# Optimization experiments

Hardware: AMD Instinct MI355X
Metric: run time of the kernel (lower is better)

Reference implementation:

```python
import jax, jax.numpy as jnp
import numpy as np

B, N, D = 2, 2048, 2048
H = 16
HD = D // H  # 128


def setup_inputs() -> dict:
    key = jax.random.key(0)
    k1, k2, k3 = jax.random.split(key, 3)
    x = jax.random.normal(k1, (B, N, D), dtype=jnp.float32)
    # Linear weights stored as [in, out] so y = x @ W matches torch's x @ W.T
    Wq = jax.random.normal(k2, (D, D), dtype=jnp.float32) * (D ** -0.5)
    Wo = jax.random.normal(k3, (D, D), dtype=jnp.float32) * (D ** -0.5)
    bo = jnp.zeros((D,), dtype=jnp.float32)
    return {"x": x, "Wq": Wq, "Wo": Wo, "bo": bo}


def reference(x, Wq, Wo, bo):
    # NOTE: source module (faithfully) projects q, k, v all with q_matrix.
    b, n, d = x.shape
    q = x @ Wq                                   # [B, N, D]
    qh = q.reshape(b, n, H, HD).transpose(0, 2, 1, 3)  # [B, H, N, HD]
    scores = jnp.einsum("bhnd,bhmd->bhnm", qh, qh) * (HD ** -0.5)  # [B,H,N,N]
    attn = jax.nn.softmax(scores, axis=-1)
    y = jnp.einsum("bhnm,bhmd->bhnd", attn, qh)  # [B, H, N, HD]
    y = y.transpose(0, 2, 1, 3).reshape(b, n, d)  # [B, N, D]
    return y @ Wo + bo
```

## Files before the change

kernel.cpp:

```cpp
#include <hip/hip_runtime.h>
#include <hip/hip_bf16.h>

#define BATCH 2
#define SEQ   2048
#define DIM   2048
#define NHEAD 16
#define HDIM  128

#define KSTRIDE 136
#define VSTRIDE 72
#define PSTRIDE 72

typedef __bf16 bf16;
typedef __attribute__((ext_vector_type(2))) __bf16 bf16x2;
typedef __attribute__((ext_vector_type(4))) __bf16 bf16x4;
typedef __attribute__((ext_vector_type(8))) __bf16 bf16x8;
typedef __attribute__((ext_vector_type(4))) float f32x4;

__device__ __forceinline__ void load_lds16(const bf16* g, bf16* l) {
    __builtin_amdgcn_global_load_lds((const __attribute__((address_space(1))) void*)g,
                                     (__attribute__((address_space(3))) void*)l, 16, 0, 0);
}

__device__ __forceinline__ float exp2_hw(float x) { return __builtin_amdgcn_exp2f(x); }

__global__ __launch_bounds__(256)
void cvt_bf16(const float* __restrict__ x, bf16* __restrict__ xb, int n4)
{
    const int i = blockIdx.x * 256 + threadIdx.x;
    if (i < n4) {
        const float4 f = ((const float4*)x)[i];
        ((bf16x4*)xb)[i] = (bf16x4){(bf16)f.x, (bf16)f.y, (bf16)f.z, (bf16)f.w};
    }
}

__global__ __launch_bounds__(256)
void transpose_w(const float* __restrict__ W, bf16* __restrict__ Wt)
{
    __shared__ bf16 T[64 * 72];
    const int kb = blockIdx.y * 64, nb = blockIdx.x * 64;

    const int a = threadIdx.x & 31;
    const int g = threadIdx.x >> 5;

    {
        const float* s0 = W + (size_t)(kb + 2 * a) * DIM + nb + g * 8;
        const float4 r0a = *(const float4*)(s0);
        const float4 r0b = *(const float4*)(s0 + 4);
        const float4 r1a = *(const float4*)(s0 + DIM);
        const float4 r1b = *(const float4*)(s0 + DIM + 4);
        float v0[8] = {r0a.x, r0a.y, r0a.z, r0a.w, r0b.x, r0b.y, r0b.z, r0b.w};
        float v1[8] = {r1a.x, r1a.y, r1a.z, r1a.w, r1b.x, r1b.y, r1b.z, r1b.w};
        #pragma unroll
        for (int i = 0; i < 8; ++i)
            *(bf16x2*)&T[(g * 8 + i) * 72 + 2 * a] = (bf16x2){(bf16)v0[i], (bf16)v1[i]};
    }
    __syncthreads();

    const int r  = threadIdx.x >> 2;
    const int k0 = (threadIdx.x & 3) * 16;
    bf16x8 o0 = *(const bf16x8*)&T[r * 72 + k0];
    bf16x8 o1 = *(const bf16x8*)&T[r * 72 + k0 + 8];
    *(bf16x8*)(Wt + (size_t)(nb + r) * DIM + kb + k0)     = o0;
    *(bf16x8*)(Wt + (size_t)(nb + r) * DIM + kb + k0 + 8) = o1;
}

template<bool OUT_F32_BIAS>
__global__ __launch_bounds__(256)
void gemm_bt(const bf16* __restrict__ A, const bf16* __restrict__ Bt,
             const float* __restrict__ bias, void* __restrict__ Cptr,
             int M, int N, int K)
{
    __shared__ bf16 As[2][128 * 32];
    __shared__ bf16 Bs[2][128 * 32];

    const int tid  = threadIdx.x;
    const int wave = tid >> 6;
    const int lane = tid & 63;
    const int quad = lane >> 4;
    const int l16  = lane & 15;
    const int wr   = (wave >> 1) * 64;
    const int wc   = (wave & 1) * 64;
    const int rowBase = blockIdx.y * 128;
    const int colBase = blockIdx.x * 128;

    const int srow = lane >> 2;
    const int scol = (lane & 3) * 8;
    const bf16* aBase = A  + (size_t)(rowBase + wave * 16 + srow) * K + scol;
    const bf16* bBase = Bt + (size_t)(colBase + wave * 16 + srow) * K + scol;

    f32x4 acc[4][4] = {};

    for (int k0 = 0; k0 < K; k0 += 64) {
        #pragma unroll
        for (int rh = 0; rh < 2; ++rh) {
            #pragma unroll
            for (int kh = 0; kh < 2; ++kh) {
                load_lds16(aBase + (size_t)rh * 64 * K + k0 + kh * 32,
                           (bf16*)As[kh] + (rh * 64 + wave * 16) * 32);
                load_lds16(bBase + (size_t)rh * 64 * K + k0 + kh * 32,
                           (bf16*)Bs[kh] + (rh * 64 + wave * 16) * 32);
            }
        }
        __syncthreads();

        #pragma unroll
        for (int ks = 0; ks < 2; ++ks) {
            bf16x8 a[4], b[4];
            #pragma unroll
            for (int i = 0; i < 4; ++i)
                a[i] = *(const bf16x8*)&As[ks][(wr + i * 16 + l16) * 32 + quad * 8];
            #pragma unroll
            for (int j = 0; j < 4; ++j)
                b[j] = *(const bf16x8*)&Bs[ks][(wc + j * 16 + l16) * 32 + quad * 8];
            #pragma unroll
            for (int i = 0; i < 4; ++i)
                #pragma unroll
                for (int j = 0; j < 4; ++j)
                    acc[i][j] = __builtin_amdgcn_mfma_f32_16x16x32_bf16(a[i], b[j], acc[i][j], 0, 0, 0);
        }
        __syncthreads();
    }

    #pragma unroll
    for (int i = 0; i < 4; ++i) {
        #pragma unroll
        for (int j = 0; j < 4; ++j) {
            #pragma unroll
            for (int r = 0; r < 4; ++r) {
                const int row = rowBase + wr + i * 16 + quad * 4 + r;
                const int col = colBase + wc + j * 16 + l16;
                const float v = acc[i][j][r];
                if (OUT_F32_BIAS) ((float*)Cptr)[(size_t)row * N + col] = v + bias[col];
                else              ((bf16*)Cptr)[(size_t)row * N + col] = (bf16)v;
            }
        }
    }
}

__global__ __launch_bounds__(256, 2)
void attn_kernel(const bf16* __restrict__ q, bf16* __restrict__ y)
{
    __shared__ bf16 Ks[64 * KSTRIDE];
    __shared__ bf16 Vt[HDIM * VSTRIDE];
    __shared__ bf16 Ps[128 * PSTRIDE];

    const int tid  = threadIdx.x;
    const int wave = tid >> 6;
    const int lane = tid & 63;
    const int quad = lane >> 4;
    const int l16  = lane & 15;

    const int qt = blockIdx.x;
    const int h  = blockIdx.y;
    const int bb = blockIdx.z;

    const bf16* qb = q + (size_t)bb * SEQ * DIM + (size_t)h * HDIM;

    const float qs = 0.12752820031096662f;
    bf16x8 aq[2][4];
    #pragma unroll
    for (int nt = 0; nt < 2; ++nt) {
        #pragma unroll
        for (int ks = 0; ks < 4; ++ks) {
            const bf16* src = qb + (size_t)(qt * 128 + wave * 32 + nt * 16 + l16) * DIM + ks * 32 + quad * 8;
            bf16x8 v = *(const bf16x8*)src;
            bf16x8 o;
            #pragma unroll
            for (int e = 0; e < 8; ++e) o[e] = (bf16)((float)v[e] * qs);
            aq[nt][ks] = o;
        }
    }

    float lpart[2] = {0.f, 0.f};
    f32x4 yacc[2][8] = {};

    const int kr   = tid >> 2;
    const int koff = (tid & 3) * 32;
    const int sp   = tid & 31;
    const int ss   = tid >> 5;

    const bf16* srcK = qb + (size_t)kr * DIM + koff;
    const bf16* srcV = qb + (size_t)(2 * sp) * DIM + ss * 16;

    bf16x8 kreg[4], va[2], vb[2];
    #pragma unroll
    for (int c = 0; c < 4; ++c) kreg[c] = *(const bf16x8*)(srcK + c * 8);
    va[0] = *(const bf16x8*)(srcV + 0);
    va[1] = *(const bf16x8*)(srcV + 8);
    vb[0] = *(const bf16x8*)(srcV + DIM + 0);
    vb[1] = *(const bf16x8*)(srcV + DIM + 8);

    for (int kt = 0; kt < SEQ / 64; ++kt) {
        __syncthreads();

        #pragma unroll
        for (int c = 0; c < 4; ++c)
            *(bf16x8*)&Ks[kr * KSTRIDE + koff + c * 8] = kreg[c];
        #pragma unroll
        for (int c = 0; c < 2; ++c)
            #pragma unroll
            for (int e = 0; e < 8; ++e)
                *(bf16x2*)&Vt[(ss * 16 + c * 8 + e) * VSTRIDE + 2 * sp] = (bf16x2){va[c][e], vb[c][e]};

        if (kt + 1 < SEQ / 64) {
            const bf16* nK = srcK + (size_t)(kt + 1) * 64 * DIM;
            const bf16* nV = srcV + (size_t)(kt + 1) * 64 * DIM;
            #pragma unroll
            for (int c = 0; c < 4; ++c) kreg[c] = *(const bf16x8*)(nK + c * 8);
            va[0] = *(const bf16x8*)(nV + 0);
            va[1] = *(const bf16x8*)(nV + 8);
            vb[0] = *(const bf16x8*)(nV + DIM + 0);
            vb[1] = *(const bf16x8*)(nV + DIM + 8);
        }
        __syncthreads();

        #pragma unroll
        for (int mt = 0; mt < 4; ++mt) {
            bf16x8 ak[4];
            #pragma unroll
            for (int ks = 0; ks < 4; ++ks)
                ak[ks] = *(const bf16x8*)&Ks[(mt * 16 + l16) * KSTRIDE + ks * 32 + quad * 8];
            f32x4 s[2] = {};
            #pragma unroll
            for (int ks = 0; ks < 4; ++ks)
                #pragma unroll
                for (int nt = 0; nt < 2; ++nt)
                    s[nt] = __builtin_amdgcn_mfma_f32_16x16x32_bf16(ak[ks], aq[nt][ks], s[nt], 0, 0, 0);
            #pragma unroll
            for (int nt = 0; nt < 2; ++nt) {
                float p0 = exp2_hw(s[nt][0]);
                float p1 = exp2_hw(s[nt][1]);
                float p2 = exp2_hw(s[nt][2]);
                float p3 = exp2_hw(s[nt][3]);
                lpart[nt] += (p0 + p1) + (p2 + p3);
                *(bf16x4*)&Ps[(wave * 32 + nt * 16 + l16) * PSTRIDE + mt * 16 + quad * 4] =
                    (bf16x4){(bf16)p0, (bf16)p1, (bf16)p2, (bf16)p3};
            }
        }

        #pragma unroll
        for (int ks2 = 0; ks2 < 2; ++ks2) {
            bf16x8 ap[2];
            #pragma unroll
            for (int i = 0; i < 2; ++i)
                ap[i] = *(const bf16x8*)&Ps[(wave * 32 + i * 16 + l16) * PSTRIDE + ks2 * 32 + quad * 8];
            #pragma unroll
            for (int n = 0; n < 8; ++n) {
                bf16x8 bv = *(const bf16x8*)&Vt[(n * 16 + l16) * VSTRIDE + ks2 * 32 + quad * 8];
                #pragma unroll
                for (int i = 0; i < 2; ++i)
                    yacc[i][n] = __builtin_amdgcn_mfma_f32_16x16x32_bf16(ap[i], bv, yacc[i][n], 0, 0, 0);
            }
        }
    }

    float lfull[2];
    #pragma unroll
    for (int nt = 0; nt < 2; ++nt) {
        float l = lpart[nt];
        l += __shfl_xor(l, 16);
        l += __shfl_xor(l, 32);
        lfull[nt] = l;
    }

    bf16* yb = y + (size_t)bb * SEQ * DIM + (size_t)(qt * 128) * DIM + (size_t)h * HDIM;
    #pragma unroll
    for (int i = 0; i < 2; ++i) {
        #pragma unroll
        for (int r = 0; r < 4; ++r) {
            const float lv  = __shfl(lfull[i], (lane & 48) | (quad * 4 + r));
            const float inv = 1.f / lv;
            const int row = wave * 32 + i * 16 + quad * 4 + r;
            #pragma unroll
            for (int n = 0; n < 8; ++n)
                yb[(size_t)row * DIM + n * 16 + l16] = (bf16)(yacc[i][n][r] * inv);
        }
    }
}

extern "C" void kernel_launch(void* const* d_in, const int* in_sizes, int n_in,
                              void* d_out, int out_size, void* d_ws, size_t ws_size,
                              hipStream_t stream)
{
    const float* x  = (const float*)d_in[0];
    const float* Wq = (const float*)d_in[1];
    const float* Wo = (const float*)d_in[2];
    const float* bo = (const float*)d_in[3];
    float* out = (float*)d_out;

    const size_t NELEM = (size_t)BATCH * SEQ * DIM;
    bf16* qws = (bf16*)d_ws;
    bf16* xb  = qws + NELEM;
    bf16* yws = xb;
    bf16* Wt  = xb + NELEM;

    const int M = BATCH * SEQ;
    dim3 gg(DIM / 128, M / 128);
    dim3 gt(DIM / 64, DIM / 64);

    cvt_bf16<<<(int)(NELEM / 4 + 255) / 256, 256, 0, stream>>>(x, xb, (int)(NELEM / 4));
    transpose_w<<<gt, 256, 0, stream>>>(Wq, Wt);
    gemm_bt<false><<<gg, 256, 0, stream>>>(xb, Wt, nullptr, qws, M, DIM, DIM);
    transpose_w<<<gt, 256, 0, stream>>>(Wo, Wt);
    attn_kernel<<<dim3(SEQ / 128, NHEAD, BATCH), 256, 0, stream>>>(qws, yws);
    gemm_bt<true><<<gg, 256, 0, stream>>>(yws, Wt, bo, out, M, DIM, DIM);
}
```

Before: 285.1 us.

## Fuse prep kernels into one launch and remap attention blocks per XCD

Merges the fp32-to-bf16 conversion of x and both weight transposes into a single prep kernel that selects its role by block index, cutting three launches down to one. The converted x is staged in the output buffer and the workspace is rearranged so both transposed weights stay resident at once. The attention grid becomes 1D, and the block index is remapped so the query tiles of a given head/batch land on the same XCD, which should improve L2 reuse of K/V. The cost is more index arithmetic, plus reliance on the output buffer being scratch until the final GEMM writes it.

```diff
diff --git a/kernel.cpp b/kernel.cpp
--- a/kernel.cpp
+++ b/kernel.cpp
@@ -25,24 +25,28 @@
 __device__ __forceinline__ float exp2_hw(float x) { return __builtin_amdgcn_exp2f(x); }
 
 __global__ __launch_bounds__(256)
-void cvt_bf16(const float* __restrict__ x, bf16* __restrict__ xb, int n4)
-{
-    const int i = blockIdx.x * 256 + threadIdx.x;
-    if (i < n4) {
-        const float4 f = ((const float4*)x)[i];
-        ((bf16x4*)xb)[i] = (bf16x4){(bf16)f.x, (bf16)f.y, (bf16)f.z, (bf16)f.w};
-    }
-}
-
-__global__ __launch_bounds__(256)
-void transpose_w(const float* __restrict__ W, bf16* __restrict__ Wt)
+void prep_kernel(const float* __restrict__ x, bf16* __restrict__ xb,
+                 const float* __restrict__ Wq, bf16* __restrict__ Wtq,
+                 const float* __restrict__ Wo, bf16* __restrict__ Wto)
 {
     __shared__ bf16 T[64 * 72];
-    const int kb = blockIdx.y * 64, nb = blockIdx.x * 64;
+    const int bid = blockIdx.x;
+    if (bid < 4096) {
+        const size_t i = ((size_t)bid * 256 + threadIdx.x) * 8;
+        const float4 f0 = *(const float4*)(x + i);
+        const float4 f1 = *(const float4*)(x + i + 4);
+        *(bf16x8*)(xb + i) = (bf16x8){(bf16)f0.x, (bf16)f0.y, (bf16)f0.z, (bf16)f0.w,
+                                      (bf16)f1.x, (bf16)f1.y, (bf16)f1.z, (bf16)f1.w};
+        return;
+    }
+    int t = bid - 4096;
+    const float* W  = (t < 1024) ? Wq : Wo;
+    bf16*        Wt = (t < 1024) ? Wtq : Wto;
+    t &= 1023;
+    const int kb = (t >> 5) * 64, nb = (t & 31) * 64;
 
     const int a = threadIdx.x & 31;
     const int g = threadIdx.x >> 5;
-
     {
         const float* s0 = W + (size_t)(kb + 2 * a) * DIM + nb + g * 8;
         const float4 r0a = *(const float4*)(s0);
@@ -151,9 +155,13 @@
     const int quad = lane >> 4;
     const int l16  = lane & 15;
 
-    const int qt = blockIdx.x;
-    const int h  = blockIdx.y;
-    const int bb = blockIdx.z;
+    const int p   = blockIdx.x;
+    const int xcd = p & 7;
+    const int pos = p >> 3;
+    const int g   = xcd * 4 + (pos & 3);
+    const int qt  = pos >> 2;
+    const int h   = g & 15;
+    const int bb  = g >> 4;
 
     const bf16* qb = q + (size_t)bb * SEQ * DIM + (size_t)h * HDIM;
 
@@ -291,18 +299,16 @@
 
     const size_t NELEM = (size_t)BATCH * SEQ * DIM;
     bf16* qws = (bf16*)d_ws;
-    bf16* xb  = qws + NELEM;
-    bf16* yws = xb;
-    bf16* Wt  = xb + NELEM;
+    bf16* yws = qws + NELEM;
+    bf16* Wtq = yws;
+    bf16* Wto = qws + 2 * NELEM;
+    bf16* xb  = (bf16*)d_out;
 
     const int M = BATCH * SEQ;
     dim3 gg(DIM / 128, M / 128);
-    dim3 gt(DIM / 64, DIM / 64);
-
-    cvt_bf16<<<(int)(NELEM / 4 + 255) / 256, 256, 0, stream>>>(x, xb, (int)(NELEM / 4));
-    transpose_w<<<gt, 256, 0, stream>>>(Wq, Wt);
-    gemm_bt<false><<<gg, 256, 0, stream>>>(xb, Wt, nullptr, qws, M, DIM, DIM);
-    transpose_w<<<gt, 256, 0, stream>>>(Wo, Wt);
-    attn_kernel<<<dim3(SEQ / 128, NHEAD, BATCH), 256, 0, stream>>>(qws, yws);
-    gemm_bt<true><<<gg, 256, 0, stream>>>(yws, Wt, bo, out, M, DIM, DIM);
-}
+
+    prep_kernel<<<6144, 256, 0, stream>>>(x, xb, Wq, Wtq, Wo, Wto);
+    gemm_bt<false><<<gg, 256, 0, stream>>>(xb, Wtq, nullptr, qws, M, DIM, DIM);
+    attn_kernel<<<512, 256, 0, stream>>>(qws, yws);
+    gemm_bt<true><<<gg, 256, 0, stream>>>(yws, Wto, bo, out, M, DIM, DIM);
+}
```

New measurement: 279.8 us. Within noise of the previous version (-1.9%).
